# Kernel optimization log

Hardware: AMD Instinct MI355X
Metric: run time of the kernel (lower is better)

## Reference

```python
import jax, jax.numpy as jnp
import numpy as np
from jax import lax

PALETTE = 256


def setup_inputs() -> dict:
    key = jax.random.key(0)
    k1, k2, k3, k4 = jax.random.split(key, 4)
    x = jax.random.normal(k1, (16, 64, 256, 256), dtype=jnp.float32)
    lookup_table = jax.random.normal(k2, (PALETTE,), dtype=jnp.float32) * 0.05
    weight_idx = jax.random.randint(k3, (64, 64, 3, 3), 0, PALETTE, dtype=jnp.int32)
    bias = jax.random.normal(k4, (64,), dtype=jnp.float32) * 0.01
    return {"x": x, "lookup_table": lookup_table, "weight_idx": weight_idx, "bias": bias}


def reference(x, lookup_table, weight_idx, bias):
    # Dequantize: palette gather produces full OIHW weight tensor.
    full_w = lookup_table[weight_idx]  # [O, I, kH, kW] float32
    # conv2d with stride=1, padding=0 (hardcoded in module), dilation=1, groups=1
    out = lax.conv_general_dilated(
        x, full_w,
        window_strides=(1, 1),
        padding='VALID',
        rhs_dilation=(1, 1),
        dimension_numbers=('NCHW', 'OIHW', 'NCHW'),
        feature_group_count=1,
    )
    return out + bias[None, :, None, None]
```

## Files before the change

kernel.cpp:

```cpp
#include <hip/hip_runtime.h>
#include <hip/hip_bf16.h>


typedef __bf16 bf16x8 __attribute__((ext_vector_type(8)));
typedef float f32x4 __attribute__((ext_vector_type(4)));

union Frag {
    uint4 q;
    bf16x8 v;
};

__global__ __launch_bounds__(256) void dequant_B(
        const float* __restrict__ lut, const int* __restrict__ widx,
        uint4* __restrict__ Bws) {
    int s = blockIdx.x * 256 + threadIdx.x;
    int l = s & 63;
    int nt = (s >> 6) & 3;
    int kc = s >> 8;
    if (kc >= 18) return;
    int r = kc >> 1;
    int kh = r / 3, kw = r - kh * 3;
    int o = nt * 16 + (l & 15);
    int c0 = (kc & 1) * 32 + (l >> 4) * 8;
    Frag f;
#pragma unroll
    for (int j = 0; j < 8; ++j) {
        int c = c0 + j;
        int idx = widx[((o * 64 + c) * 3 + kh) * 3 + kw];
        f.v[j] = (__bf16)lut[idx];
    }
    Bws[s] = f.q;
}

#define LDS_PIX 396

__global__ __launch_bounds__(256, 3) void conv_mfma(
        const float* __restrict__ x, const float* __restrict__ bias,
        const uint4* __restrict__ Bws, float* __restrict__ out) {
    __shared__ uint4 ldsA[8 * LDS_PIX];

    int bx = blockIdx.x;
    int ow0 = (bx & 3) * 64;
    int oh0 = ((bx >> 2) & 63) * 4;
    int n = bx >> 8;
    int t = threadIdx.x;

    {
        const float* xn = x + (size_t)n * (64 * 256 * 256);
        int col = t & 63;
        int cbb = t >> 6;
#pragma unroll
        for (int cp = 0; cp < 2; ++cp) {
            int cblk = cbb + cp * 4;
#pragma unroll
            for (int rr = 0; rr < 6; ++rr) {
                int y = oh0 + rr; if (y > 255) y = 255;
                const float* src = xn + cblk * 8 * 65536 + y * 256 + ow0 + col;
                Frag f;
#pragma unroll
                for (int j = 0; j < 8; ++j)
                    f.v[j] = (__bf16)src[j * 65536];
                ldsA[cblk * LDS_PIX + rr * 66 + col] = f.q;
            }
        }
        if (t < 96) {
            int cblk = t & 7;
            int rc = t >> 3;
            int rr = rc >> 1;
            int col2 = 64 + (rc & 1);
            int y = oh0 + rr; if (y > 255) y = 255;
            int xc = ow0 + col2; if (xc > 255) xc = 255;
            const float* src = xn + cblk * 8 * 65536 + y * 256 + xc;
            Frag f;
#pragma unroll
            for (int j = 0; j < 8; ++j)
                f.v[j] = (__bf16)src[j * 65536];
            ldsA[cblk * LDS_PIX + rr * 66 + col2] = f.q;
        }
    }
    __syncthreads();

    int w = t >> 6;
    int l = t & 63;
    int l15 = l & 15, l4 = l >> 4;

    f32x4 acc[4][4] = {};

    for (int kc = 0; kc < 18; ++kc) {
        int r = kc >> 1;
        int kh = r / 3, kw = r - kh * 3;
        int cblk = (kc & 1) * 4 + l4;
        int pix = (w + kh) * 66 + l15 + kw;

        Frag b[4];
#pragma unroll
        for (int nt = 0; nt < 4; ++nt)
            b[nt].q = Bws[(kc * 4 + nt) * 64 + l];

        Frag a[4];
#pragma unroll
        for (int mt = 0; mt < 4; ++mt)
            a[mt].q = ldsA[cblk * LDS_PIX + pix + mt * 16];

#pragma unroll
        for (int mt = 0; mt < 4; ++mt)
#pragma unroll
            for (int nt = 0; nt < 4; ++nt)
                acc[mt][nt] = __builtin_amdgcn_mfma_f32_16x16x32_bf16(
                    a[mt].v, b[nt].v, acc[mt][nt], 0, 0, 0);
    }

    int oh = oh0 + w;
    if (oh < 254) {
#pragma unroll
        for (int nt = 0; nt < 4; ++nt) {
            int o = nt * 16 + l15;
            float bv = bias[o];
            float* obase = out + (((size_t)n * 64 + o) * 254 + oh) * 254 + ow0;
#pragma unroll
            for (int mt = 0; mt < 4; ++mt) {
#pragma unroll
                for (int rg = 0; rg < 4; ++rg) {
                    int owl = mt * 16 + l4 * 4 + rg;
                    if (ow0 + owl < 254)
                        obase[owl] = acc[mt][nt][rg] + bv;
                }
            }
        }
    }
}

extern "C" void kernel_launch(void* const* d_in, const int* in_sizes, int n_in,
                              void* d_out, int out_size, void* d_ws, size_t ws_size,
                              hipStream_t stream) {
    const float* x    = (const float*)d_in[0];
    const float* lut  = (const float*)d_in[1];
    const int*   widx = (const int*)d_in[2];
    const float* bias = (const float*)d_in[3];
    float* out = (float*)d_out;
    uint4* Bws = (uint4*)d_ws;

    dequant_B<<<18, 256, 0, stream>>>(lut, widx, Bws);
    conv_mfma<<<4096, 256, 0, stream>>>(x, bias, (const uint4*)Bws, out);
}
```

Before: 519.1 us.

## Use 512-thread blocks with swapped MFMA operands and pixel-major output stores

```diff
diff --git a/kernel.cpp b/kernel.cpp
--- a/kernel.cpp
+++ b/kernel.cpp
@@ -10,17 +10,17 @@
     bf16x8 v;
 };
 
-__global__ __launch_bounds__(256) void dequant_B(
+__global__ __launch_bounds__(256) void dequant_W(
         const float* __restrict__ lut, const int* __restrict__ widx,
-        uint4* __restrict__ Bws) {
-    int s = blockIdx.x * 256 + threadIdx.x;
-    int l = s & 63;
-    int nt = (s >> 6) & 3;
-    int kc = s >> 8;
+        uint4* __restrict__ Wg) {
+    int g = blockIdx.x * 256 + threadIdx.x;
+    int l = g & 63;
+    int mt = (g >> 6) & 3;
+    int kc = g >> 8;
     if (kc >= 18) return;
     int r = kc >> 1;
     int kh = r / 3, kw = r - kh * 3;
-    int o = nt * 16 + (l & 15);
+    int o = mt * 16 + (l & 15);
     int c0 = (kc & 1) * 32 + (l >> 4) * 8;
     Frag f;
 #pragma unroll
@@ -29,14 +29,14 @@
         int idx = widx[((o * 64 + c) * 3 + kh) * 3 + kw];
         f.v[j] = (__bf16)lut[idx];
     }
-    Bws[s] = f.q;
+    Wg[g] = f.q;
 }
 
 #define LDS_PIX 396
 
-__global__ __launch_bounds__(256, 3) void conv_mfma(
+__global__ __launch_bounds__(512, 6) void conv_mfma(
         const float* __restrict__ x, const float* __restrict__ bias,
-        const uint4* __restrict__ Bws, float* __restrict__ out) {
+        const uint4* __restrict__ Wg, float* __restrict__ out) {
     __shared__ uint4 ldsA[8 * LDS_PIX];
 
     int bx = blockIdx.x;
@@ -48,34 +48,31 @@
     {
         const float* xn = x + (size_t)n * (64 * 256 * 256);
         int col = t & 63;
-        int cbb = t >> 6;
+        int cblk = t >> 6;
+        const float* base = xn + cblk * 8 * 65536 + ow0 + col;
 #pragma unroll
-        for (int cp = 0; cp < 2; ++cp) {
-            int cblk = cbb + cp * 4;
+        for (int rr = 0; rr < 6; ++rr) {
+            int y = oh0 + rr; if (y > 255) y = 255;
+            const float* src = base + y * 256;
+            Frag f;
 #pragma unroll
-            for (int rr = 0; rr < 6; ++rr) {
-                int y = oh0 + rr; if (y > 255) y = 255;
-                const float* src = xn + cblk * 8 * 65536 + y * 256 + ow0 + col;
-                Frag f;
-#pragma unroll
-                for (int j = 0; j < 8; ++j)
-                    f.v[j] = (__bf16)src[j * 65536];
-                ldsA[cblk * LDS_PIX + rr * 66 + col] = f.q;
-            }
+            for (int j = 0; j < 8; ++j)
+                f.v[j] = (__bf16)src[j * 65536];
+            ldsA[cblk * LDS_PIX + rr * 66 + col] = f.q;
         }
         if (t < 96) {
-            int cblk = t & 7;
+            int cb = t & 7;
             int rc = t >> 3;
             int rr = rc >> 1;
             int col2 = 64 + (rc & 1);
             int y = oh0 + rr; if (y > 255) y = 255;
             int xc = ow0 + col2; if (xc > 255) xc = 255;
-            const float* src = xn + cblk * 8 * 65536 + y * 256 + xc;
+            const float* src = xn + cb * 8 * 65536 + y * 256 + xc;
             Frag f;
 #pragma unroll
             for (int j = 0; j < 8; ++j)
                 f.v[j] = (__bf16)src[j * 65536];
-            ldsA[cblk * LDS_PIX + rr * 66 + col2] = f.q;
+            ldsA[cb * LDS_PIX + rr * 66 + col2] = f.q;
         }
     }
     __syncthreads();
@@ -83,47 +80,54 @@
     int w = t >> 6;
     int l = t & 63;
     int l15 = l & 15, l4 = l >> 4;
+    int ohl = w >> 1;
+    int owh = (w & 1) * 32;
 
-    f32x4 acc[4][4] = {};
+    f32x4 acc[4][2] = {};
 
+    const uint4* Wl = Wg + l;
+
+#pragma unroll
     for (int kc = 0; kc < 18; ++kc) {
-        int r = kc >> 1;
-        int kh = r / 3, kw = r - kh * 3;
-        int cblk = (kc & 1) * 4 + l4;
-        int pix = (w + kh) * 66 + l15 + kw;
+        const int h = kc & 1;
+        const int r = kc >> 1;
+        const int kh = r / 3, kw = r - kh * 3;
+        int rowcol = (ohl + kh) * 66 + owh + l15 + kw;
+        int cb = (h * 4 + l4) * LDS_PIX;
 
-        Frag b[4];
-#pragma unroll
-        for (int nt = 0; nt < 4; ++nt)
-            b[nt].q = Bws[(kc * 4 + nt) * 64 + l];
+        Frag b[2];
+        b[0].q = ldsA[cb + rowcol];
+        b[1].q = ldsA[cb + rowcol + 16];
 
         Frag a[4];
 #pragma unroll
         for (int mt = 0; mt < 4; ++mt)
-            a[mt].q = ldsA[cblk * LDS_PIX + pix + mt * 16];
+            a[mt].q = Wl[(kc * 4 + mt) * 64];
 
 #pragma unroll
         for (int mt = 0; mt < 4; ++mt)
 #pragma unroll
-            for (int nt = 0; nt < 4; ++nt)
+            for (int nt = 0; nt < 2; ++nt)
                 acc[mt][nt] = __builtin_amdgcn_mfma_f32_16x16x32_bf16(
                     a[mt].v, b[nt].v, acc[mt][nt], 0, 0, 0);
     }
 
-    int oh = oh0 + w;
+    int oh = oh0 + ohl;
     if (oh < 254) {
+        const float* outn = out + (size_t)n * (64 * 254 * 254);
+        int owB = ow0 + owh + l15;
 #pragma unroll
-        for (int nt = 0; nt < 4; ++nt) {
-            int o = nt * 16 + l15;
-            float bv = bias[o];
-            float* obase = out + (((size_t)n * 64 + o) * 254 + oh) * 254 + ow0;
+        for (int nt = 0; nt < 2; ++nt) {
+            int ow = owB + nt * 16;
+            if (ow < 254) {
 #pragma unroll
-            for (int mt = 0; mt < 4; ++mt) {
+                for (int mt = 0; mt < 4; ++mt) {
 #pragma unroll
-                for (int rg = 0; rg < 4; ++rg) {
-                    int owl = mt * 16 + l4 * 4 + rg;
-                    if (ow0 + owl < 254)
-                        obase[owl] = acc[mt][nt][rg] + bv;
+                    for (int rg = 0; rg < 4; ++rg) {
+                        int o = mt * 16 + l4 * 4 + rg;
+                        ((float*)outn)[(size_t)o * (254 * 254) + oh * 254 + ow] =
+                            acc[mt][nt][rg] + bias[o];
+                    }
                 }
             }
         }
@@ -138,8 +142,8 @@
     const int*   widx = (const int*)d_in[2];
     const float* bias = (const float*)d_in[3];
     float* out = (float*)d_out;
-    uint4* Bws = (uint4*)d_ws;
+    uint4* Wg = (uint4*)d_ws;
 
-    dequant_B<<<18, 256, 0, stream>>>(lut, widx, Bws);
-    conv_mfma<<<4096, 256, 0, stream>>>(x, bias, (const uint4*)Bws, out);
+    dequant_W<<<18, 256, 0, stream>>>(lut, widx, Wg);
+    conv_mfma<<<4096, 512, 0, stream>>>(x, bias, (const uint4*)Wg, out);
 }
```

After: 573.3 us. 10.4% more time.
